# Kernel optimization log

Measured on AMD Instinct MI355X. Metric: run time of the kernel, lower is better.

## Reference

```python
import jax, jax.numpy as jnp
import numpy as np


def setup_inputs() -> dict:
    key = jax.random.key(0)
    ks = jax.random.split(key, 4)
    L, B, T, H, D = 12, 4, 2048, 16, 64
    current_layer = jax.random.normal(ks[0], (B, T, H, D), dtype=jnp.float32)
    all_layers = jax.random.normal(ks[1], (L, B, T, H, D), dtype=jnp.float32)
    # nn.init.normal_(std=0.02) for both projections
    Wq = jax.random.normal(ks[2], (D, D), dtype=jnp.float32) * 0.02
    Wk = jax.random.normal(ks[3], (D, D), dtype=jnp.float32) * 0.02
    scales = jnp.full((L,), 1.0 / L, dtype=jnp.float32)  # LayerScalingFactor init 1/num_layers
    temperature = jnp.ones((1,), dtype=jnp.float32)
    return {
        "current_layer": current_layer,
        "all_layers": all_layers,
        "Wq": Wq,
        "Wk": Wk,
        "scales": scales,
        "temperature": temperature,
        "current_layer_idx": 0,
    }


def reference(current_layer, all_layers, Wq, Wk, scales, temperature, current_layer_idx):
    # current_layer: [B,T,H,D]; all_layers: [L,B,T,H,D] (stack of per-layer outputs)
    # num_heads = 1, so per-head dim == D and scores are over the layer axis L.
    D = current_layer.shape[-1]
    q = jnp.einsum("bthd,ed->bthe", current_layer, Wq)          # query_proj (no bias)
    k = jnp.einsum("lbthd,ed->lbthe", all_layers, Wk)           # key_proj (no bias)
    inv_scale = 1.0 / (jnp.sqrt(jnp.asarray(D, q.dtype)) * jnp.abs(temperature[0]))
    scores = jnp.einsum("bthd,lbthd->bthl", q, k) * inv_scale   # [B,T,H,L]
    attn = jax.nn.softmax(scores, axis=-1)
    attn = attn * scales                                        # per-layer learned scale
    attn = attn / (jnp.sum(attn, axis=-1, keepdims=True) + 1e-6)  # renormalize
    # per-layer accumulation: output += scales[l] * attn[...,l] * all_layers[l]
    out = jnp.einsum("bthl,l,lbthd->bthd", attn, scales, all_layers)
    return out
```

## Files before the change

### kernel.cpp

```cpp
#include <hip/hip_runtime.h>
#include <hip/hip_bf16.h>

constexpr int L = 12;
constexpr int B = 4, T = 2048, H = 16, D = 64;
constexpr int NPOS = B * T * H;
constexpr long long SLAYER = (long long)NPOS * D;
constexpr int PW = 16;

typedef __attribute__((ext_vector_type(8))) short bf16x8;
typedef __attribute__((ext_vector_type(4))) float f32x4;

__device__ __forceinline__ short f2bf(float f) {
  union { __hip_bfloat16 h; short s; } u;
  u.h = __float2bfloat16(f);
  return u.s;
}

__global__ __launch_bounds__(64) void cla_precompute_MT(
    const float* __restrict__ Wq, const float* __restrict__ Wk,
    short* __restrict__ MT) {
  const int n = blockIdx.x;
  const int k = threadIdx.x;
  float acc = 0.f;
  #pragma unroll
  for (int e = 0; e < D; ++e)
    acc = fmaf(Wq[e * D + k], Wk[e * D + n], acc);
  MT[n * D + k] = f2bf(acc);
}

template <int CTRL>
__device__ __forceinline__ float ror_add(float x) {
  int moved = __builtin_amdgcn_update_dpp(0, __float_as_int(x), CTRL, 0xF, 0xF,
                                          false);
  return x + __int_as_float(moved);
}
__device__ __forceinline__ float row_sum16(float x) {
  x = ror_add<0x121>(x);
  x = ror_add<0x122>(x);
  x = ror_add<0x124>(x);
  x = ror_add<0x128>(x);
  return x;
}

__global__ __launch_bounds__(256, 3) void cla_main(
    const float* __restrict__ cur, const float* __restrict__ all,
    const short* __restrict__ MT, const float* __restrict__ scales,
    const float* __restrict__ temperature, float* __restrict__ out) {
  __shared__ float qlds[4][PW * D];

  const int lane = threadIdx.x & 63;
  const int w    = threadIdx.x >> 6;
  const int wid  = blockIdx.x * 4 + w;
  const int pos0 = wid * PW;

  const int ncol = lane & 15;
  const int kq   = lane >> 4;

  bf16x8 bm[4][2];
  #pragma unroll
  for (int nt = 0; nt < 4; ++nt)
    #pragma unroll
    for (int kc = 0; kc < 2; ++kc)
      bm[nt][kc] =
          *(const bf16x8*)(MT + (nt * 16 + ncol) * D + kc * 32 + kq * 8);

  f32x4 acc[4] = {};
  const float* xb = cur + (size_t)(pos0 + ncol) * D + kq * 8;
  #pragma unroll
  for (int kc = 0; kc < 2; ++kc) {
    const float4 xlo = *(const float4*)(xb + kc * 32);
    const float4 xhi = *(const float4*)(xb + kc * 32 + 4);
    short a8[8] = {f2bf(xlo.x), f2bf(xlo.y), f2bf(xlo.z), f2bf(xlo.w),
                   f2bf(xhi.x), f2bf(xhi.y), f2bf(xhi.z), f2bf(xhi.w)};
    bf16x8 af;
    __builtin_memcpy(&af, a8, 16);
    #pragma unroll
    for (int nt = 0; nt < 4; ++nt)
      acc[nt] = __builtin_amdgcn_mfma_f32_16x16x32_bf16(af, bm[nt][kc],
                                                        acc[nt], 0, 0, 0);
  }

  const float inv_scale = 1.0f / (8.0f * fabsf(temperature[0]));

  #pragma unroll
  for (int nt = 0; nt < 4; ++nt)
    #pragma unroll
    for (int r = 0; r < 4; ++r)
      qlds[w][(4 * kq + r) * D + nt * 16 + ncol] = acc[nt][r] * inv_scale;

  float scl[L];
  #pragma unroll
  for (int l = 0; l < L; ++l) scl[l] = scales[l];

  const int g = lane >> 4;
  const int j = lane & 15;

  for (int it = 0; it < 4; ++it) {
    const size_t base = (size_t)(pos0 + it * 4) * D + (size_t)lane * 4;
    const float4 q = *(const float4*)&qlds[w][(it * 4 + g) * D + 4 * j];

    float4 y[L];
    #pragma unroll
    for (int l = 0; l < L; ++l)
      y[l] = *(const float4*)(all + (size_t)l * SLAYER + base);

    float sc[L];
    #pragma unroll
    for (int l = 0; l < L; ++l) {
      float s = q.x * y[l].x + q.y * y[l].y + q.z * y[l].z + q.w * y[l].w;
      sc[l] = row_sum16(s);
    }

    float mx = sc[0];
    #pragma unroll
    for (int l = 1; l < L; ++l) mx = fmaxf(mx, sc[l]);
    float sum = 0.f;
    #pragma unroll
    for (int l = 0; l < L; ++l) { sc[l] = __expf(sc[l] - mx); sum += sc[l]; }
    const float inv_sum = 1.0f / sum;

    float wgt[L];
    float ssum = 0.f;
    #pragma unroll
    for (int l = 0; l < L; ++l) {
      wgt[l] = sc[l] * inv_sum * scl[l];
      ssum += wgt[l];
    }
    const float r = 1.0f / (ssum + 1e-6f);

    float o0 = 0.f, o1 = 0.f, o2 = 0.f, o3 = 0.f;
    #pragma unroll
    for (int l = 0; l < L; ++l) {
      const float wl = wgt[l] * r * scl[l];
      o0 = fmaf(wl, y[l].x, o0);
      o1 = fmaf(wl, y[l].y, o1);
      o2 = fmaf(wl, y[l].z, o2);
      o3 = fmaf(wl, y[l].w, o3);
    }
    *(float4*)(out + base) = make_float4(o0, o1, o2, o3);
  }
}

extern "C" void kernel_launch(void* const* d_in, const int* in_sizes, int n_in,
                              void* d_out, int out_size, void* d_ws, size_t ws_size,
                              hipStream_t stream) {
  const float* cur    = (const float*)d_in[0];
  const float* all    = (const float*)d_in[1];
  const float* Wq     = (const float*)d_in[2];
  const float* Wk     = (const float*)d_in[3];
  const float* scales = (const float*)d_in[4];
  const float* temp   = (const float*)d_in[5];
  short* MT = (short*)d_ws;

  cla_precompute_MT<<<64, 64, 0, stream>>>(Wq, Wk, MT);

  const int nwaves  = NPOS / PW;
  const int nblocks = nwaves / 4;
  cla_main<<<nblocks, 256, 0, stream>>>(cur, all, MT, scales, temp,
                                        (float*)d_out);
}
```

Before: 105.6 us.

## Process one position per wave iteration with full-wave reduction and higher occupancy

The main loop now handles one position per iteration, with each lane holding one scalar element instead of a float4. A wave-wide DPP row_shr/row_bcast reduction plus readlane replaces the 16-lane row sums. The B-matrix fragments are loaded per tile instead of held live, and scales are read from memory directly, all to cut register pressure so launch bounds can ask for 8 blocks per SIMD instead of 3. The trade is scalar 4-byte loads instead of 16-byte vector loads on a bandwidth-bound stream, a longer serial reduction chain per score, and more loop iterations.

```diff
diff --git a/kernel.cpp b/kernel.cpp
--- a/kernel.cpp
+++ b/kernel.cpp
@@ -28,21 +28,23 @@
   MT[n * D + k] = f2bf(acc);
 }
 
-template <int CTRL>
-__device__ __forceinline__ float ror_add(float x) {
-  int moved = __builtin_amdgcn_update_dpp(0, __float_as_int(x), CTRL, 0xF, 0xF,
+template <int CTRL, int ROWM>
+__device__ __forceinline__ float dpp_add(float x) {
+  int moved = __builtin_amdgcn_update_dpp(0, __float_as_int(x), CTRL, ROWM, 0xF,
                                           false);
   return x + __int_as_float(moved);
 }
-__device__ __forceinline__ float row_sum16(float x) {
-  x = ror_add<0x121>(x);
-  x = ror_add<0x122>(x);
-  x = ror_add<0x124>(x);
-  x = ror_add<0x128>(x);
-  return x;
+__device__ __forceinline__ float wave_sum_bcast(float x) {
+  x = dpp_add<0x111, 0xF>(x);
+  x = dpp_add<0x112, 0xF>(x);
+  x = dpp_add<0x114, 0xF>(x);
+  x = dpp_add<0x118, 0xF>(x);
+  x = dpp_add<0x142, 0xA>(x);
+  x = dpp_add<0x143, 0xC>(x);
+  return __int_as_float(__builtin_amdgcn_readlane(__float_as_int(x), 63));
 }
 
-__global__ __launch_bounds__(256, 3) void cla_main(
+__global__ __launch_bounds__(256, 8) void cla_main(
     const float* __restrict__ cur, const float* __restrict__ all,
     const short* __restrict__ MT, const float* __restrict__ scales,
     const float* __restrict__ temperature, float* __restrict__ out) {
@@ -56,60 +58,50 @@
   const int ncol = lane & 15;
   const int kq   = lane >> 4;
 
-  bf16x8 bm[4][2];
-  #pragma unroll
-  for (int nt = 0; nt < 4; ++nt)
+  const float inv_scale = 1.0f / (8.0f * fabsf(temperature[0]));
+
+  bf16x8 af[2];
+  {
+    const float* xb = cur + (size_t)(pos0 + ncol) * D + kq * 8;
     #pragma unroll
-    for (int kc = 0; kc < 2; ++kc)
-      bm[nt][kc] =
-          *(const bf16x8*)(MT + (nt * 16 + ncol) * D + kc * 32 + kq * 8);
-
-  f32x4 acc[4] = {};
-  const float* xb = cur + (size_t)(pos0 + ncol) * D + kq * 8;
-  #pragma unroll
-  for (int kc = 0; kc < 2; ++kc) {
-    const float4 xlo = *(const float4*)(xb + kc * 32);
-    const float4 xhi = *(const float4*)(xb + kc * 32 + 4);
-    short a8[8] = {f2bf(xlo.x), f2bf(xlo.y), f2bf(xlo.z), f2bf(xlo.w),
-                   f2bf(xhi.x), f2bf(xhi.y), f2bf(xhi.z), f2bf(xhi.w)};
-    bf16x8 af;
-    __builtin_memcpy(&af, a8, 16);
-    #pragma unroll
-    for (int nt = 0; nt < 4; ++nt)
-      acc[nt] = __builtin_amdgcn_mfma_f32_16x16x32_bf16(af, bm[nt][kc],
-                                                        acc[nt], 0, 0, 0);
+    for (int kc = 0; kc < 2; ++kc) {
+      const float4 xlo = *(const float4*)(xb + kc * 32);
+      const float4 xhi = *(const float4*)(xb + kc * 32 + 4);
+      short a8[8] = {f2bf(xlo.x), f2bf(xlo.y), f2bf(xlo.z), f2bf(xlo.w),
+                     f2bf(xhi.x), f2bf(xhi.y), f2bf(xhi.z), f2bf(xhi.w)};
+      __builtin_memcpy(&af[kc], a8, 16);
+    }
   }
 
-  const float inv_scale = 1.0f / (8.0f * fabsf(temperature[0]));
-
   #pragma unroll
-  for (int nt = 0; nt < 4; ++nt)
+  for (int nt = 0; nt < 4; ++nt) {
+    f32x4 acc = {};
+    #pragma unroll
+    for (int kc = 0; kc < 2; ++kc) {
+      const bf16x8 bm =
+          *(const bf16x8*)(MT + (nt * 16 + ncol) * D + kc * 32 + kq * 8);
+      acc = __builtin_amdgcn_mfma_f32_16x16x32_bf16(af[kc], bm, acc, 0, 0, 0);
+    }
     #pragma unroll
     for (int r = 0; r < 4; ++r)
-      qlds[w][(4 * kq + r) * D + nt * 16 + ncol] = acc[nt][r] * inv_scale;
+      qlds[w][(4 * kq + r) * D + nt * 16 + ncol] = acc[r] * inv_scale;
+  }
 
-  float scl[L];
-  #pragma unroll
-  for (int l = 0; l < L; ++l) scl[l] = scales[l];
+  for (int it = 0; it < PW; ++it) {
+    const size_t pbase = (size_t)(pos0 + it) * D;
+    const float q = qlds[w][it * D + lane];
 
-  const int g = lane >> 4;
-  const int j = lane & 15;
-
-  for (int it = 0; it < 4; ++it) {
-    const size_t base = (size_t)(pos0 + it * 4) * D + (size_t)lane * 4;
-    const float4 q = *(const float4*)&qlds[w][(it * 4 + g) * D + 4 * j];
-
-    float4 y[L];
+    float y[L];
     #pragma unroll
-    for (int l = 0; l < L; ++l)
-      y[l] = *(const float4*)(all + (size_t)l * SLAYER + base);
+    for (int l = 0; l < L; ++l) {
+      const float* p = all + (size_t)l * SLAYER + pbase;
+      y[l] = p[lane];
+    }
 
     float sc[L];
     #pragma unroll
-    for (int l = 0; l < L; ++l) {
-      float s = q.x * y[l].x + q.y * y[l].y + q.z * y[l].z + q.w * y[l].w;
-      sc[l] = row_sum16(s);
-    }
+    for (int l = 0; l < L; ++l)
+      sc[l] = wave_sum_bcast(q * y[l]);
 
     float mx = sc[0];
     #pragma unroll
@@ -119,25 +111,19 @@
     for (int l = 0; l < L; ++l) { sc[l] = __expf(sc[l] - mx); sum += sc[l]; }
     const float inv_sum = 1.0f / sum;
 
-    float wgt[L];
     float ssum = 0.f;
     #pragma unroll
     for (int l = 0; l < L; ++l) {
-      wgt[l] = sc[l] * inv_sum * scl[l];
-      ssum += wgt[l];
+      sc[l] = sc[l] * inv_sum * scales[l];
+      ssum += sc[l];
     }
     const float r = 1.0f / (ssum + 1e-6f);
 
-    float o0 = 0.f, o1 = 0.f, o2 = 0.f, o3 = 0.f;
+    float o = 0.f;
     #pragma unroll
-    for (int l = 0; l < L; ++l) {
-      const float wl = wgt[l] * r * scl[l];
-      o0 = fmaf(wl, y[l].x, o0);
-      o1 = fmaf(wl, y[l].y, o1);
-      o2 = fmaf(wl, y[l].z, o2);
-      o3 = fmaf(wl, y[l].w, o3);
-    }
-    *(float4*)(out + base) = make_float4(o0, o1, o2, o3);
+    for (int l = 0; l < L; ++l) o = fmaf(sc[l] * r * scales[l], y[l], o);
+
+    out[pbase + lane] = o;
   }
 }
 
```

After: 113.9 us. 1.08x slower.
